# Kernel optimization log

Hardware: AMD Instinct MI355X
Metric: run time of the kernel (lower is better)

Reference implementation:

```python
import jax, jax.numpy as jnp
import numpy as np

B = 100_000   # graph nodes in batch
C = 1_000     # virtual-node clusters
D = 512       # in_dim (attention hidden dim)
OUT = 512     # out_dim


def setup_inputs() -> dict:
    key = jax.random.key(0)
    ks = jax.random.split(key, 9)
    h = jax.random.normal(ks[0], (B, D), dtype=jnp.float32)
    g = jax.random.normal(ks[1], (C, D), dtype=jnp.float32)
    # vn_index[:,1] is the cluster id of node i; arange%C guarantees every
    # cluster is present, so the per-cluster concat has exactly C rows in
    # sorted-cluster-id order (matching torch .unique() iteration order).
    vn_index = jnp.stack([jnp.arange(B, dtype=jnp.int32),
                          jnp.arange(B, dtype=jnp.int32) % C], axis=1)
    n_id = jnp.arange(B, dtype=jnp.int32)
    s = 1.0 / np.sqrt(D)
    Wq = jax.random.uniform(ks[2], (D, D), jnp.float32, -s, s)   # query_proj (no bias)
    Wk = jax.random.uniform(ks[3], (D, D), jnp.float32, -s, s)   # key_proj (no bias)
    attn_bias = jax.random.uniform(ks[4], (D,), jnp.float32, -0.1, 0.1)
    Ws = jax.random.uniform(ks[5], (1, D), jnp.float32, -s, s)   # score_proj weight
    bs = jax.random.uniform(ks[6], (1,), jnp.float32, -s, s)     # score_proj bias
    so = 1.0 / np.sqrt(D)
    W = jax.random.uniform(ks[7], (OUT, D), jnp.float32, -so, so)  # final Linear
    b = jax.random.uniform(ks[8], (OUT,), jnp.float32, -so, so)
    return {"h": h, "g": g, "vn_index": vn_index, "n_id": n_id,
            "Wq": Wq, "Wk": Wk, "attn_bias": attn_bias, "Ws": Ws, "bs": bs,
            "W": W, "b": b}


def reference(h, g, vn_index, n_id, Wq, Wk, attn_bias, Ws, bs, W, b):
    # cluster id for each batch node (B,)
    cluster = vn_index[n_id, 1]
    # additive attention, vectorized over all nodes (replaces per-cluster loop)
    qp = g @ Wq.T                                   # (C, D) query proj per cluster
    kp = h @ Wk.T                                   # (B, D) key proj per node
    score = jnp.tanh(kp + qp[cluster] + attn_bias) @ Ws[0] + bs[0]  # (B,)
    # segment softmax over each cluster
    smax = jax.ops.segment_max(score, cluster, num_segments=C)      # (C,)
    e = jnp.exp(score - smax[cluster])                              # (B,)
    denom = jax.ops.segment_sum(e, cluster, num_segments=C)         # (C,)
    attn = e / denom[cluster]                                       # (B,)
    # attention-weighted sum of node features per cluster -> (C, D)
    ctx = jax.ops.segment_sum(attn[:, None] * h, cluster, num_segments=C)
    # final projection + tanh activation -> (C, OUT)
    return jnp.tanh(ctx @ W.T + b)
```

## Files before the change

kernel.cpp:

```cpp
#include <hip/hip_runtime.h>
#include <stdint.h>

#define D_DIM 512

typedef __attribute__((ext_vector_type(8))) short bf16x8;
typedef __attribute__((ext_vector_type(4))) float f32x4;
typedef __attribute__((ext_vector_type(4))) short short4_t;
typedef __attribute__((ext_vector_type(4))) float float4_t;

__device__ __forceinline__ unsigned short f2bf(float f) {
  unsigned u = __float_as_uint(f);
  u += 0x7FFFu + ((u >> 16) & 1u);
  return (unsigned short)(u >> 16);
}

__device__ __forceinline__ float bf2f(unsigned short s) {
  return __uint_as_float(((unsigned)s) << 16);
}

__device__ __forceinline__ float tanh_fast(float x) {
  float e = __expf(2.0f * x);
  return 1.0f - 2.0f / (e + 1.0f);
}

#define GLOAD_LDS16(gsrc, ldst) \
  __builtin_amdgcn_global_load_lds((const __attribute__((address_space(1))) void*)(gsrc), \
                                   (__attribute__((address_space(3))) void*)(ldst), 16, 0, 0)


__global__ void cvt_f32_bf16_k(const float* __restrict__ in, unsigned short* __restrict__ out, int n4) {
  int i = blockIdx.x * blockDim.x + threadIdx.x;
  if (i < n4) {
    float4_t v = ((const float4_t*)in)[i];
    short4_t s;
    s.x = (short)f2bf(v.x); s.y = (short)f2bf(v.y);
    s.z = (short)f2bf(v.z); s.w = (short)f2bf(v.w);
    ((short4_t*)out)[i] = s;
  }
}

__global__ void cvt3_f32_bf16_k(const float* __restrict__ a, const float* __restrict__ b,
                                const float* __restrict__ c, unsigned short* __restrict__ out,
                                int n4each) {
  int i = blockIdx.x * blockDim.x + threadIdx.x;
  if (i >= 3 * n4each) return;
  int sel = i / n4each, j = i - sel * n4each;
  const float* src = (sel == 0) ? a : (sel == 1) ? b : c;
  float4_t v = ((const float4_t*)src)[j];
  short4_t s;
  s.x = (short)f2bf(v.x); s.y = (short)f2bf(v.y);
  s.z = (short)f2bf(v.z); s.w = (short)f2bf(v.w);
  ((short4_t*)out)[i] = s;
}

__global__ void prep_cluster_k(const int* __restrict__ vn, const int* __restrict__ nid,
                               int* __restrict__ cl, int* __restrict__ counts, int B) {
  int i = blockIdx.x * blockDim.x + threadIdx.x;
  if (i < B) {
    int c = vn[2 * nid[i] + 1];
    cl[i] = c;
    atomicAdd(&counts[c], 1);
  }
}

__global__ void prefix_k(const int* __restrict__ counts, int* __restrict__ starts,
                         int* __restrict__ cursor, int C) {
  __shared__ int sh[1024];
  int t = threadIdx.x;
  int v = (t < C) ? counts[t] : 0;
  sh[t] = v;
  __syncthreads();
  for (int off = 1; off < 1024; off <<= 1) {
    int x = (t >= off) ? sh[t - off] : 0;
    __syncthreads();
    sh[t] += x;
    __syncthreads();
  }
  if (t < C) { int st = sh[t] - v; starts[t] = st; cursor[t] = st; }
  if (t == 1023) starts[C] = sh[1023];
}

__global__ void scatter_k(const int* __restrict__ cl, int* __restrict__ cursor,
                          int* __restrict__ order, int B) {
  int i = blockIdx.x * blockDim.x + threadIdx.x;
  if (i < B) {
    int pos = atomicAdd(&cursor[cl[i]], 1);
    order[pos] = i;
  }
}

__device__ __forceinline__ unsigned enc_f(float f) {
  unsigned u = __float_as_uint(f);
  return (u & 0x80000000u) ? ~u : (u | 0x80000000u);
}
__device__ __forceinline__ float dec_f(unsigned u) {
  return __uint_as_float((u & 0x80000000u) ? (u & 0x7FFFFFFFu) : ~u);
}

__global__ void seg_max_k(const float* __restrict__ score, const int* __restrict__ cl,
                          unsigned* __restrict__ smax, int B) {
  int i = blockIdx.x * blockDim.x + threadIdx.x;
  if (i < B) atomicMax(&smax[cl[i]], enc_f(score[i]));
}

__global__ void seg_expsum_k(const float* __restrict__ score, const int* __restrict__ cl,
                             const unsigned* __restrict__ smax, float* __restrict__ ev,
                             float* __restrict__ denom, int B) {
  int i = blockIdx.x * blockDim.x + threadIdx.x;
  if (i < B) {
    int c = cl[i];
    float x = __expf(score[i] - dec_f(smax[c]));
    ev[i] = x;
    atomicAdd(&denom[c], x);
  }
}

__global__ __launch_bounds__(256)
void ctx_k(const unsigned short* __restrict__ hbf, const float* __restrict__ ev,
           const int* __restrict__ order, const int* __restrict__ starts,
           const float* __restrict__ denom, float* __restrict__ ctx) {
  int c = blockIdx.x;
  int t = threadIdx.x;
  int s0 = starts[c], s1 = starts[c + 1];
  float a0 = 0.f, a1 = 0.f;
  int j = s0;
  for (; j + 3 < s1; j += 4) {
    int i0 = order[j], i1 = order[j + 1], i2 = order[j + 2], i3 = order[j + 3];
    float e0 = ev[i0], e1 = ev[i1], e2 = ev[i2], e3 = ev[i3];
    unsigned u0 = *(const unsigned*)(hbf + (size_t)i0 * D_DIM + t * 2);
    unsigned u1 = *(const unsigned*)(hbf + (size_t)i1 * D_DIM + t * 2);
    unsigned u2 = *(const unsigned*)(hbf + (size_t)i2 * D_DIM + t * 2);
    unsigned u3 = *(const unsigned*)(hbf + (size_t)i3 * D_DIM + t * 2);
    a0 += e0 * bf2f((unsigned short)u0) + e1 * bf2f((unsigned short)u1)
        + e2 * bf2f((unsigned short)u2) + e3 * bf2f((unsigned short)u3);
    a1 += e0 * bf2f((unsigned short)(u0 >> 16)) + e1 * bf2f((unsigned short)(u1 >> 16))
        + e2 * bf2f((unsigned short)(u2 >> 16)) + e3 * bf2f((unsigned short)(u3 >> 16));
  }
  for (; j < s1; ++j) {
    int i0 = order[j];
    float e0 = ev[i0];
    unsigned u0 = *(const unsigned*)(hbf + (size_t)i0 * D_DIM + t * 2);
    a0 += e0 * bf2f((unsigned short)u0);
    a1 += e0 * bf2f((unsigned short)(u0 >> 16));
  }
  float inv = 1.0f / denom[c];
  float2 r = make_float2(a0 * inv, a1 * inv);
  *(float2*)(&ctx[(size_t)c * D_DIM + t * 2]) = r;
}

__global__ __launch_bounds__(512, 2)
void gemm256_score_k(const unsigned short* __restrict__ Abf,
                     const unsigned short* __restrict__ Bw, int M,
                     const float* __restrict__ qb, const int* __restrict__ cl,
                     const float* __restrict__ Ws, float* __restrict__ out)
{
  __shared__ unsigned short AB[65536];
  __shared__ float red[256][4];
  __shared__ int clds[256];

  const int t = threadIdx.x;
  const int lane = t & 63;
  const int w = t >> 6;
  const int wr = w >> 2, wc = w & 3;
  const int l15 = lane & 15, l4 = lane >> 4;

  const int nwg = gridDim.x;
  {
  }
  int id;
  {
    int q = nwg >> 3, r = nwg & 7;
    int xcd = blockIdx.x & 7, pos = blockIdx.x >> 3;
    id = (xcd < r ? xcd * (q + 1) : r * (q + 1) + (xcd - r) * q) + pos;
  }
  const int n0 = (id & 1) * 256;
  const int m0 = (id >> 1) * 256;

  if (t < 256) {
    int gm = m0 + t;
    clds[t] = (gm < M) ? cl[gm < M ? gm : M - 1] : cl[M - 1];
  }
  __builtin_amdgcn_sched_barrier(0);

  const int rin = lane >> 3;
  const int sl = lane & 7;
  const int sslot = sl ^ rin;

  const unsigned short* srcA[4];
  const unsigned short* srcB[4];
  int chunkOff[4];
  #pragma unroll
  for (int c = 0; c < 4; ++c) {
    int chunk = w * 4 + c;
    int rowA = m0 + chunk * 8 + rin; if (rowA > M - 1) rowA = M - 1;
    int colB = n0 + chunk * 8 + rin;
    srcA[c] = Abf + (size_t)rowA * 512 + sslot * 8;
    srcB[c] = Bw + (size_t)colB * 512 + sslot * 8;
    chunkOff[c] = chunk * 1024;
  }

  int rowA_off[8], rowB_off[4];
  #pragma unroll
  for (int mi = 0; mi < 8; ++mi) rowA_off[mi] = (wr * 128 + mi * 16 + l15) * 128;
  #pragma unroll
  for (int ni = 0; ni < 4; ++ni) rowB_off[ni] = (wc * 64 + ni * 16 + l15) * 128;
  int psk[2];
  psk[0] = ((l4) ^ (l15 & 7)) * 16;
  psk[1] = ((4 + l4) ^ (l15 & 7)) * 16;

  f32x4 acc[8][4];
  #pragma unroll
  for (int mi = 0; mi < 8; ++mi)
    #pragma unroll
    for (int ni = 0; ni < 4; ++ni)
      acc[mi][ni] = (f32x4){0.f, 0.f, 0.f, 0.f};

  #pragma unroll
  for (int c = 0; c < 4; ++c)
    GLOAD_LDS16(srcA[c], ((char*)AB) + chunkOff[c]);
  #pragma unroll
  for (int c = 0; c < 4; ++c)
    GLOAD_LDS16(srcB[c], ((char*)AB) + 65536 + chunkOff[c]);
  __builtin_amdgcn_sched_barrier(0);

  #pragma unroll
  for (int kt = 0; kt < 8; ++kt) {
    const int buf = kt & 1;
    const char* Au = ((const char*)AB) + buf * 32768;
    const char* Bu = ((const char*)AB) + 65536 + buf * 32768;
    char* AuN = ((char*)AB) + (buf ^ 1) * 32768;
    char* BuN = ((char*)AB) + 65536 + (buf ^ 1) * 32768;

    asm volatile("s_waitcnt vmcnt(0)" ::: "memory");
    __builtin_amdgcn_sched_barrier(0);
    __builtin_amdgcn_s_barrier();
    __builtin_amdgcn_sched_barrier(0);

    #pragma unroll
    for (int ks = 0; ks < 2; ++ks) {
      bf16x8 a[8], b[4];
      #pragma unroll
      for (int mi = 0; mi < 8; ++mi)
        a[mi] = *(const bf16x8*)(Au + rowA_off[mi] + psk[ks]);
      #pragma unroll
      for (int ni = 0; ni < 4; ++ni)
        b[ni] = *(const bf16x8*)(Bu + rowB_off[ni] + psk[ks]);

      if (kt < 7) {
        const int k1 = (kt + 1) * 64;
        if (ks == 0) {
          #pragma unroll
          for (int c = 0; c < 4; ++c)
            GLOAD_LDS16(srcA[c] + k1, AuN + chunkOff[c]);
        } else {
          #pragma unroll
          for (int c = 0; c < 4; ++c)
            GLOAD_LDS16(srcB[c] + k1, BuN + chunkOff[c]);
        }
      }
      __builtin_amdgcn_sched_barrier(0);

      __builtin_amdgcn_s_setprio(1);
      #pragma unroll
      for (int mi = 0; mi < 8; ++mi)
        #pragma unroll
        for (int ni = 0; ni < 4; ++ni)
          acc[mi][ni] = __builtin_amdgcn_mfma_f32_16x16x32_bf16(a[mi], b[ni], acc[mi][ni], 0, 0, 0);
      __builtin_amdgcn_s_setprio(0);
      __builtin_amdgcn_sched_barrier(0);

      if (ks == 0) {
        __builtin_amdgcn_s_barrier();
        __builtin_amdgcn_sched_barrier(0);
      }
    }
  }

  __syncthreads();
  #pragma unroll
  for (int mi = 0; mi < 8; ++mi) {
    #pragma unroll
    for (int r = 0; r < 4; ++r) {
      int rowt = wr * 128 + mi * 16 + l4 * 4 + r;
      int c = clds[rowt];
      const float* qrow = &qb[(size_t)c * 512];
      float s = 0.f;
      #pragma unroll
      for (int ni = 0; ni < 4; ++ni) {
        int gcol = n0 + wc * 64 + ni * 16 + l15;
        float x = acc[mi][ni][r] + qrow[gcol];
        s += tanh_fast(x) * Ws[gcol];
      }
      s += __shfl_xor(s, 1);
      s += __shfl_xor(s, 2);
      s += __shfl_xor(s, 4);
      s += __shfl_xor(s, 8);
      if (l15 == 0) red[rowt][wc] = s;
    }
  }
  __syncthreads();
  if (t < 256) {
    int gm = m0 + t;
    if (gm < M) atomicAdd(&out[gm], red[t][0] + red[t][1] + red[t][2] + red[t][3]);
  }
}

template<int EPI>
__global__ __launch_bounds__(256)
void gemm128_k(const unsigned short* __restrict__ Abf,
               const unsigned short* __restrict__ Bw, int M,
               const float* __restrict__ bias, float* __restrict__ out)
{
  __shared__ unsigned short As[2][128 * 32];
  __shared__ unsigned short Bs[2][128 * 32];

  const int t = threadIdx.x;
  const int lane = t & 63;
  const int w = t >> 6;
  const int wr = w >> 1, wc = w & 1;
  const int l15 = lane & 15, l4 = lane >> 4;

  const int nwg = gridDim.x;
  int id = blockIdx.x;
  if ((nwg & 7) == 0) id = (id & 7) * (nwg >> 3) + (id >> 3);
  const int n0 = (id & 3) * 128;
  const int m0 = (id >> 2) * 128;

  const int rin = lane >> 2;
  const int sl = lane & 3;

  const unsigned short* srcA[2];
  const unsigned short* srcB[2];
  int dstOff[2];
  #pragma unroll
  for (int c = 0; c < 2; ++c) {
    int chunk = w * 2 + c;
    int row = chunk * 16 + rin;
    int slot = sl ^ ((row ^ (row >> 2)) & 3);
    int ga = m0 + row; if (ga > M - 1) ga = M - 1;
    srcA[c] = Abf + (size_t)ga * 512 + slot * 8;
    srcB[c] = Bw + (size_t)(n0 + row) * 512 + slot * 8;
    dstOff[c] = chunk * 1024;
  }

  int offA[4], offB[4];
  #pragma unroll
  for (int mi = 0; mi < 4; ++mi) {
    int row = wr * 64 + mi * 16 + l15;
    offA[mi] = row * 64 + ((l4 ^ ((row ^ (row >> 2)) & 3)) * 16);
  }
  #pragma unroll
  for (int ni = 0; ni < 4; ++ni) {
    int row = wc * 64 + ni * 16 + l15;
    offB[ni] = row * 64 + ((l4 ^ ((row ^ (row >> 2)) & 3)) * 16);
  }

  f32x4 acc[4][4];
  #pragma unroll
  for (int mi = 0; mi < 4; ++mi)
    #pragma unroll
    for (int ni = 0; ni < 4; ++ni)
      acc[mi][ni] = (f32x4){0.f, 0.f, 0.f, 0.f};

  #pragma unroll
  for (int c = 0; c < 2; ++c) {
    GLOAD_LDS16(srcA[c], ((char*)As[0]) + dstOff[c]);
    GLOAD_LDS16(srcB[c], ((char*)Bs[0]) + dstOff[c]);
  }
  __builtin_amdgcn_sched_barrier(0);

  #pragma unroll
  for (int it = 0; it < 16; ++it) {
    const int cur = it & 1;
    if (it < 15) {
      const int k1 = (it + 1) * 32;
      #pragma unroll
      for (int c = 0; c < 2; ++c) {
        GLOAD_LDS16(srcA[c] + k1, ((char*)As[cur ^ 1]) + dstOff[c]);
        GLOAD_LDS16(srcB[c] + k1, ((char*)Bs[cur ^ 1]) + dstOff[c]);
      }
      __builtin_amdgcn_sched_barrier(0);
      asm volatile("s_waitcnt vmcnt(4)" ::: "memory");
    } else {
      asm volatile("s_waitcnt vmcnt(0)" ::: "memory");
    }
    __builtin_amdgcn_sched_barrier(0);
    __builtin_amdgcn_s_barrier();
    __builtin_amdgcn_sched_barrier(0);

    {
      bf16x8 af[4], bfv[4];
      #pragma unroll
      for (int mi = 0; mi < 4; ++mi)
        af[mi] = *(const bf16x8*)(((const char*)As[cur]) + offA[mi]);
      #pragma unroll
      for (int ni = 0; ni < 4; ++ni)
        bfv[ni] = *(const bf16x8*)(((const char*)Bs[cur]) + offB[ni]);
      #pragma unroll
      for (int mi = 0; mi < 4; ++mi)
        #pragma unroll
        for (int ni = 0; ni < 4; ++ni)
          acc[mi][ni] = __builtin_amdgcn_mfma_f32_16x16x32_bf16(af[mi], bfv[ni], acc[mi][ni], 0, 0, 0);
    }
    __builtin_amdgcn_sched_barrier(0);
    __builtin_amdgcn_s_barrier();
    __builtin_amdgcn_sched_barrier(0);
  }

  #pragma unroll
  for (int mi = 0; mi < 4; ++mi) {
    #pragma unroll
    for (int r = 0; r < 4; ++r) {
      int gm = m0 + wr * 64 + mi * 16 + l4 * 4 + r;
      if (gm < M) {
        #pragma unroll
        for (int ni = 0; ni < 4; ++ni) {
          int gcol = n0 + wc * 64 + ni * 16 + l15;
          float v = acc[mi][ni][r] + bias[gcol];
          if (EPI == 2) v = tanh_fast(v);
          out[(size_t)gm * 512 + gcol] = v;
        }
      }
    }
  }
}


extern "C" void kernel_launch(void* const* d_in, const int* in_sizes, int n_in,
                              void* d_out, int out_size, void* d_ws, size_t ws_size,
                              hipStream_t stream) {
  const float* h  = (const float*)d_in[0];
  const float* g  = (const float*)d_in[1];
  const int*   vn = (const int*)d_in[2];
  const int*   nid= (const int*)d_in[3];
  const float* Wq = (const float*)d_in[4];
  const float* Wk = (const float*)d_in[5];
  const float* ab = (const float*)d_in[6];
  const float* Ws = (const float*)d_in[7];
  const float* W  = (const float*)d_in[9];
  const float* b  = (const float*)d_in[10];

  const int B = in_sizes[3];
  const int C = in_sizes[1] / D_DIM;

  char* wsb = (char*)d_ws;
  size_t off = 0;
  auto alloc = [&](size_t bytes) -> void* {
    void* p = wsb + off;
    off += (bytes + 255) & ~(size_t)255;
    return p;
  };

  unsigned short* hbf   = (unsigned short*)alloc((size_t)B * 512 * 2);
  unsigned short* gbf   = (unsigned short*)alloc((size_t)C * 512 * 2);
  unsigned short* ctxbf = (unsigned short*)alloc((size_t)C * 512 * 2);
  unsigned short* Wk_bf = (unsigned short*)alloc((size_t)512 * 512 * 2);
  unsigned short* Wq_bf = (unsigned short*)alloc((size_t)512 * 512 * 2);
  unsigned short* W_bf  = (unsigned short*)alloc((size_t)512 * 512 * 2);
  float* qb    = (float*)alloc((size_t)C * 512 * 4);
  float* ctx   = (float*)alloc((size_t)C * 512 * 4);
  float* score = (float*)alloc((size_t)B * 4);
  float* ev    = (float*)alloc((size_t)B * 4);
  int*   cl    = (int*)alloc((size_t)B * 4);
  int*   order = (int*)alloc((size_t)B * 4);
  int*      counts = (int*)alloc((size_t)C * 4);
  unsigned* smax   = (unsigned*)alloc((size_t)C * 4);
  float*    denom  = (float*)alloc((size_t)C * 4);
  int* starts = (int*)alloc((size_t)(C + 1) * 4);
  int* cursor = (int*)alloc((size_t)C * 4);
  (void)ws_size; (void)n_in; (void)out_size;

  size_t zlen = (size_t)((char*)denom - (char*)counts) + (size_t)C * 4;
  hipMemsetAsync(counts, 0, zlen, stream);
  hipMemsetAsync(score, 0, (size_t)B * 4, stream);

  cvt_f32_bf16_k<<<(B * 512 / 4 + 255) / 256, 256, 0, stream>>>(h, hbf, B * 512 / 4);
  cvt_f32_bf16_k<<<(C * 512 / 4 + 255) / 256, 256, 0, stream>>>(g, gbf, C * 512 / 4);
  const int n4w = 512 * 512 / 4;
  cvt3_f32_bf16_k<<<(3 * n4w + 255) / 256, 256, 0, stream>>>(Wk, Wq, W, Wk_bf, n4w);

  prep_cluster_k<<<(B + 255) / 256, 256, 0, stream>>>(vn, nid, cl, counts, B);
  prefix_k<<<1, 1024, 0, stream>>>(counts, starts, cursor, C);
  scatter_k<<<(B + 255) / 256, 256, 0, stream>>>(cl, cursor, order, B);

  gemm128_k<0><<<4 * ((C + 127) / 128), 256, 0, stream>>>(gbf, Wq_bf, C, ab, qb);

  gemm256_score_k<<<2 * ((B + 255) / 256), 512, 0, stream>>>(
      hbf, Wk_bf, B, qb, cl, Ws, score);

  seg_max_k<<<(B + 255) / 256, 256, 0, stream>>>(score, cl, smax, B);
  seg_expsum_k<<<(B + 255) / 256, 256, 0, stream>>>(score, cl, smax, ev, denom, B);
  ctx_k<<<C, 256, 0, stream>>>(hbf, ev, order, starts, denom, ctx);

  cvt_f32_bf16_k<<<(C * 512 / 4 + 255) / 256, 256, 0, stream>>>(ctx, ctxbf, C * 512 / 4);

  gemm128_k<2><<<4 * ((C + 127) / 128), 256, 0, stream>>>(ctxbf, W_bf, C, b, (float*)d_out);
}
```

Baseline: 248.8 us.

## Shrink score GEMM tile to 256x128 with single-buffered LDS loads

Replaces the 256x256 double-buffered score GEMM with a 256x128 tile that loads each K slice synchronously into a single LDS buffer. The grid doubles so N is split into four 128-wide column tiles, each doing its own partial tanh-score reduction via atomics. This cuts LDS and accumulator-register use to allow more concurrent workgroups per CU, at the cost of losing the software prefetch overlap and reading the A operand twice as often.

```diff
diff --git a/kernel.cpp b/kernel.cpp
--- a/kernel.cpp
+++ b/kernel.cpp
@@ -148,89 +148,93 @@
   *(float2*)(&ctx[(size_t)c * D_DIM + t * 2]) = r;
 }
 
-__global__ __launch_bounds__(512, 2)
-void gemm256_score_k(const unsigned short* __restrict__ Abf,
-                     const unsigned short* __restrict__ Bw, int M,
-                     const float* __restrict__ qb, const int* __restrict__ cl,
-                     const float* __restrict__ Ws, float* __restrict__ out)
+__global__ __launch_bounds__(512)
+void gemm256x128_score_k(const unsigned short* __restrict__ Abf,
+                         const unsigned short* __restrict__ Bw, int M,
+                         const float* __restrict__ qb, const int* __restrict__ cl,
+                         const float* __restrict__ Ws, float* __restrict__ out)
 {
-  __shared__ unsigned short AB[65536];
-  __shared__ float red[256][4];
+  __shared__ unsigned short AB[24576];
+  __shared__ float red[256][2];
   __shared__ int clds[256];
 
   const int t = threadIdx.x;
   const int lane = t & 63;
   const int w = t >> 6;
-  const int wr = w >> 2, wc = w & 3;
+  const int wr = w >> 1, wc = w & 1;
   const int l15 = lane & 15, l4 = lane >> 4;
 
-  const int nwg = gridDim.x;
-  {
-  }
   int id;
   {
+    int nwg = gridDim.x;
     int q = nwg >> 3, r = nwg & 7;
     int xcd = blockIdx.x & 7, pos = blockIdx.x >> 3;
     id = (xcd < r ? xcd * (q + 1) : r * (q + 1) + (xcd - r) * q) + pos;
   }
-  const int n0 = (id & 1) * 256;
-  const int m0 = (id >> 1) * 256;
+  const int n0 = (id & 3) * 128;
+  const int m0 = (id >> 2) * 256;
 
   if (t < 256) {
     int gm = m0 + t;
-    clds[t] = (gm < M) ? cl[gm < M ? gm : M - 1] : cl[M - 1];
-  }
-  __builtin_amdgcn_sched_barrier(0);
+    clds[t] = cl[gm < M ? gm : M - 1];
+  }
+  asm volatile("s_waitcnt lgkmcnt(0)" ::: "memory");
 
   const int rin = lane >> 3;
-  const int sl = lane & 7;
-  const int sslot = sl ^ rin;
+  const int ss = (lane & 7) ^ rin;
 
   const unsigned short* srcA[4];
-  const unsigned short* srcB[4];
-  int chunkOff[4];
+  int dstA[4];
   #pragma unroll
   for (int c = 0; c < 4; ++c) {
     int chunk = w * 4 + c;
     int rowA = m0 + chunk * 8 + rin; if (rowA > M - 1) rowA = M - 1;
+    srcA[c] = Abf + (size_t)rowA * 512 + ss * 8;
+    dstA[c] = chunk * 1024;
+  }
+  const unsigned short* srcB[2];
+  int dstB[2];
+  #pragma unroll
+  for (int c = 0; c < 2; ++c) {
+    int chunk = w * 2 + c;
     int colB = n0 + chunk * 8 + rin;
-    srcA[c] = Abf + (size_t)rowA * 512 + sslot * 8;
-    srcB[c] = Bw + (size_t)colB * 512 + sslot * 8;
-    chunkOff[c] = chunk * 1024;
-  }
-
-  int rowA_off[8], rowB_off[4];
-  #pragma unroll
-  for (int mi = 0; mi < 8; ++mi) rowA_off[mi] = (wr * 128 + mi * 16 + l15) * 128;
-  #pragma unroll
-  for (int ni = 0; ni < 4; ++ni) rowB_off[ni] = (wc * 64 + ni * 16 + l15) * 128;
-  int psk[2];
-  psk[0] = ((l4) ^ (l15 & 7)) * 16;
-  psk[1] = ((4 + l4) ^ (l15 & 7)) * 16;
-
-  f32x4 acc[8][4];
-  #pragma unroll
-  for (int mi = 0; mi < 8; ++mi)
+    srcB[c] = Bw + (size_t)colB * 512 + ss * 8;
+    dstB[c] = 32768 + chunk * 1024;
+  }
+
+  int offA[4][2], offB[4][2];
+  #pragma unroll
+  for (int mi = 0; mi < 4; ++mi) {
+    int row = wr * 64 + mi * 16 + l15;
+    #pragma unroll
+    for (int ks = 0; ks < 2; ++ks)
+      offA[mi][ks] = row * 128 + (((ks * 4 + l4) ^ (row & 7)) * 16);
+  }
+  #pragma unroll
+  for (int ni = 0; ni < 4; ++ni) {
+    int row = wc * 64 + ni * 16 + l15;
+    #pragma unroll
+    for (int ks = 0; ks < 2; ++ks)
+      offB[ni][ks] = 32768 + row * 128 + (((ks * 4 + l4) ^ (row & 7)) * 16);
+  }
+
+  f32x4 acc[4][4];
+  #pragma unroll
+  for (int mi = 0; mi < 4; ++mi)
     #pragma unroll
     for (int ni = 0; ni < 4; ++ni)
       acc[mi][ni] = (f32x4){0.f, 0.f, 0.f, 0.f};
 
   #pragma unroll
-  for (int c = 0; c < 4; ++c)
-    GLOAD_LDS16(srcA[c], ((char*)AB) + chunkOff[c]);
-  #pragma unroll
-  for (int c = 0; c < 4; ++c)
-    GLOAD_LDS16(srcB[c], ((char*)AB) + 65536 + chunkOff[c]);
-  __builtin_amdgcn_sched_barrier(0);
-
-  #pragma unroll
   for (int kt = 0; kt < 8; ++kt) {
-    const int buf = kt & 1;
-    const char* Au = ((const char*)AB) + buf * 32768;
-    const char* Bu = ((const char*)AB) + 65536 + buf * 32768;
-    char* AuN = ((char*)AB) + (buf ^ 1) * 32768;
-    char* BuN = ((char*)AB) + 65536 + (buf ^ 1) * 32768;
-
+    const int k1 = kt * 64;
+    #pragma unroll
+    for (int c = 0; c < 4; ++c)
+      GLOAD_LDS16(srcA[c] + k1, ((char*)AB) + dstA[c]);
+    #pragma unroll
+    for (int c = 0; c < 2; ++c)
+      GLOAD_LDS16(srcB[c] + k1, ((char*)AB) + dstB[c]);
+    __builtin_amdgcn_sched_barrier(0);
     asm volatile("s_waitcnt vmcnt(0)" ::: "memory");
     __builtin_amdgcn_sched_barrier(0);
     __builtin_amdgcn_s_barrier();
@@ -238,50 +242,31 @@
 
     #pragma unroll
     for (int ks = 0; ks < 2; ++ks) {
-      bf16x8 a[8], b[4];
-      #pragma unroll
-      for (int mi = 0; mi < 8; ++mi)
-        a[mi] = *(const bf16x8*)(Au + rowA_off[mi] + psk[ks]);
+      bf16x8 a[4], b[4];
+      #pragma unroll
+      for (int mi = 0; mi < 4; ++mi)
+        a[mi] = *(const bf16x8*)(((const char*)AB) + offA[mi][ks]);
       #pragma unroll
       for (int ni = 0; ni < 4; ++ni)
-        b[ni] = *(const bf16x8*)(Bu + rowB_off[ni] + psk[ks]);
-
-      if (kt < 7) {
-        const int k1 = (kt + 1) * 64;
-        if (ks == 0) {
-          #pragma unroll
-          for (int c = 0; c < 4; ++c)
-            GLOAD_LDS16(srcA[c] + k1, AuN + chunkOff[c]);
-        } else {
-          #pragma unroll
-          for (int c = 0; c < 4; ++c)
-            GLOAD_LDS16(srcB[c] + k1, BuN + chunkOff[c]);
-        }
-      }
-      __builtin_amdgcn_sched_barrier(0);
-
+        b[ni] = *(const bf16x8*)(((const char*)AB) + offB[ni][ks]);
       __builtin_amdgcn_s_setprio(1);
       #pragma unroll
-      for (int mi = 0; mi < 8; ++mi)
+      for (int mi = 0; mi < 4; ++mi)
         #pragma unroll
         for (int ni = 0; ni < 4; ++ni)
           acc[mi][ni] = __builtin_amdgcn_mfma_f32_16x16x32_bf16(a[mi], b[ni], acc[mi][ni], 0, 0, 0);
       __builtin_amdgcn_s_setprio(0);
-      __builtin_amdgcn_sched_barrier(0);
-
-      if (ks == 0) {
-        __builtin_amdgcn_s_barrier();
-        __builtin_amdgcn_sched_barrier(0);
-      }
     }
-  }
-
-  __syncthreads();
-  #pragma unroll
-  for (int mi = 0; mi < 8; ++mi) {
+    __builtin_amdgcn_sched_barrier(0);
+    __builtin_amdgcn_s_barrier();
+    __builtin_amdgcn_sched_barrier(0);
+  }
+
+  #pragma unroll
+  for (int mi = 0; mi < 4; ++mi) {
     #pragma unroll
     for (int r = 0; r < 4; ++r) {
-      int rowt = wr * 128 + mi * 16 + l4 * 4 + r;
+      int rowt = wr * 64 + mi * 16 + l4 * 4 + r;
       int c = clds[rowt];
       const float* qrow = &qb[(size_t)c * 512];
       float s = 0.f;
@@ -301,7 +286,7 @@
   __syncthreads();
   if (t < 256) {
     int gm = m0 + t;
-    if (gm < M) atomicAdd(&out[gm], red[t][0] + red[t][1] + red[t][2] + red[t][3]);
+    if (gm < M) atomicAdd(&out[gm], red[t][0] + red[t][1]);
   }
 }
 
@@ -485,7 +470,7 @@
 
   gemm128_k<0><<<4 * ((C + 127) / 128), 256, 0, stream>>>(gbf, Wq_bf, C, ab, qb);
 
-  gemm256_score_k<<<2 * ((B + 255) / 256), 512, 0, stream>>>(
+  gemm256x128_score_k<<<4 * ((B + 255) / 256), 512, 0, stream>>>(
       hbf, Wk_bf, B, qb, cl, Ws, score);
 
   seg_max_k<<<(B + 255) / 256, 256, 0, stream>>>(score, cl, smax, B);
```

New measurement: 272.4 us. 1.09x slower.
